# Optimization experiments

Measured on AMD Instinct MI355X. Metric: run time of the kernel, lower is better.

The kernel has to match this reference:

```python
import jax, jax.numpy as jnp
import numpy as np


def _conv3x3(x, w, b):
    # x: [B,C,H,W], w: [O,C,3,3], b: [O]; stride 1, padding 1 (SAME)
    y = jax.lax.conv_general_dilated(
        x, w, window_strides=(1, 1), padding='SAME',
        dimension_numbers=('NCHW', 'OIHW', 'NCHW'))
    return y + b[None, :, None, None]


def setup_inputs() -> dict:
    key = jax.random.key(0)
    ks = jax.random.split(key, 7)
    B, C, H, W = 8, 256, 48, 48
    emb = 512
    fan_out = emb * 9  # kaiming_normal_ fan_out, relu gain sqrt(2)
    std = float(np.sqrt(2.0 / fan_out))
    feat = jax.random.normal(ks[0], (B, C, H, W), dtype=jnp.float32)
    Wq = jax.random.normal(ks[1], (emb, C, 3, 3), dtype=jnp.float32) * std
    Wk = jax.random.normal(ks[2], (emb, C, 3, 3), dtype=jnp.float32) * std
    Wv = jax.random.normal(ks[3], (emb, C, 3, 3), dtype=jnp.float32) * std
    bound = 1.0 / np.sqrt(C * 9)
    bq = jax.random.uniform(ks[4], (emb,), jnp.float32, -bound, bound)
    bk = jax.random.uniform(ks[5], (emb,), jnp.float32, -bound, bound)
    bv = jax.random.uniform(ks[6], (emb,), jnp.float32, -bound, bound)
    return {"feat": feat, "Wq": Wq, "bq": bq, "Wk": Wk, "bk": bk, "Wv": Wv, "bv": bv}


def reference(feat, Wq, bq, Wk, bk, Wv, bv):
    B, C, H, W = feat.shape
    emb = Wq.shape[0]
    q = _conv3x3(feat, Wq, bq).reshape(B, emb, H * W)  # [B,E,N]
    k = _conv3x3(feat, Wk, bk).reshape(B, emb, H * W)
    v = _conv3x3(feat, Wv, bv).reshape(B, emb, H * W)
    # att[b,i,j] = <q[:, i], k[:, j]>, softmax over j (keys)
    att = jnp.einsum('bei,bej->bij', q, k)
    att = jax.nn.softmax(att, axis=2)
    # v_att[b,e,i] = sum_j v[b,e,j] * att[b,i,j]
    v_att = jnp.einsum('bej,bij->bei', v, att)
    return v_att.reshape(B, emb, H, W) + v.reshape(B, emb, H, W)
```

## Files before the change

### kernel.cpp

```cpp
#include <hip/hip_runtime.h>


typedef _Float16 f16;
typedef _Float16 f16x4 __attribute__((ext_vector_type(4)));
typedef _Float16 f16x8 __attribute__((ext_vector_type(8)));
typedef float    f32x4  __attribute__((ext_vector_type(4)));
typedef float    f32x16 __attribute__((ext_vector_type(16)));

__device__ __forceinline__ f32x16 mfma16(f16x8 a, f16x8 b, f32x16 c) {
  return __builtin_amdgcn_mfma_f32_32x32x16_f16(a, b, c, 0, 0, 0);
}

#define NB   8
#define NC   256
#define NH   48
#define NN   2304
#define NE   512
#define HP   50


__global__ void pack_feat(const float* __restrict__ x, f16* __restrict__ p) {
  int idx = blockIdx.x * 256 + threadIdx.x;
  int c  = idx & 255;
  int q  = idx >> 8;
  int xp = q % 50; int t = q / 50; int yp = t % 50; int b = t / 50;
  float v = 0.f;
  if (yp >= 1 && yp <= 48 && xp >= 1 && xp <= 48)
    v = x[((b * NC + c) * NH + (yp - 1)) * NH + (xp - 1)];
  p[idx] = (f16)v;
}

__global__ void pack_w(const float* __restrict__ wq, const float* __restrict__ wk,
                       const float* __restrict__ wv,
                       f16* __restrict__ oq, f16* __restrict__ ok,
                       f16* __restrict__ ov) {
  int idx = blockIdx.x * 256 + threadIdx.x;
  int c = idx & 255;
  int r = idx >> 8;
  int e = r & 511; int t = r >> 9;
  int src = (e * NC + c) * 9 + t;
  int cc = c >> 4, cl = c & 15, et = e >> 5, el = e & 31;
  int dst = ((cc * 9 + t) * 16 + et) * 512 + el * 16 + cl;
  oq[dst] = (f16)wq[src];
  ok[dst] = (f16)wk[src];
  ov[dst] = (f16)wv[src];
}

__global__ __launch_bounds__(256, 3) void conv3_all(
    const f16* __restrict__ xh,
    const f16* __restrict__ wq, const f16* __restrict__ wk,
    const f16* __restrict__ wv,
    const float* __restrict__ bq, const float* __restrict__ bk,
    const float* __restrict__ bv,
    f16* __restrict__ oq, f16* __restrict__ okf, f16* __restrict__ ovf) {
  __shared__ __align__(16) f16 sx[2][12000];

  const int tid = threadIdx.x;
  const int lane = tid & 63, wvx = tid >> 6;
  const int l31 = lane & 31;
  const int koff = (lane >> 5) * 8;
  const int et = blockIdx.x;
  const int e0 = et * 32;
  const int by = blockIdx.y;
  const int b = by / 6, strip = by % 6;
  const int y0 = strip * 8;
  const int F = blockIdx.z;
  const f16* w = (F == 0) ? wq : (F == 1) ? wk : wv;
  const float* bias = (F == 0) ? bq : (F == 1) ? bk : bv;

  int pb[3];
#pragma unroll
  for (int nt = 0; nt < 3; ++nt) {
    int n = wvx * 96 + nt * 32 + l31;
    pb[nt] = (n / 48) * 50 + (n % 48);
  }

  int sgp[4], sgo[4]; bool sok[4]; int gbase[4];
#pragma unroll
  for (int u = 0; u < 4; ++u) {
    int g = u * 256 + tid;
    sok[u] = (g < 1000);
    int gg = sok[u] ? g : 999;
    sgp[u] = gg >> 1; sgo[u] = (gg & 1) * 8;
    int row = sgp[u] / 50, xx = sgp[u] % 50;
    gbase[u] = ((b * HP + y0 + row) * HP + xx) * NC + sgo[u];
  }

  f32x16 acc[3];
#pragma unroll
  for (int nt = 0; nt < 3; ++nt)
#pragma unroll
    for (int i = 0; i < 16; ++i) acc[nt][i] = 0.f;

  const int wlocal = l31 * 16 + koff;

  {
    f16x8 rx0[4];
#pragma unroll
    for (int u = 0; u < 4; ++u)
      rx0[u] = *(const f16x8*)(xh + gbase[u]);
#pragma unroll
    for (int u = 0; u < 4; ++u)
      if (sok[u]) *(f16x8*)(sx[0] + sgp[u] * 24 + sgo[u]) = rx0[u];
  }
  __syncthreads();

  for (int cc = 0; cc < 16; ++cc) {
    f16x8 rx[4];
    if (cc < 15) {
      int c0 = (cc + 1) * 16;
#pragma unroll
      for (int u = 0; u < 4; ++u)
        rx[u] = *(const f16x8*)(xh + gbase[u] + c0);
    }
    const f16* sxc = sx[cc & 1];
    f16x8 wf = *(const f16x8*)(w + ((cc * 9 + 0) * 16 + et) * 512 + wlocal);
#pragma unroll
    for (int t = 0; t < 9; ++t) {
      f16x8 wcur = wf;
      if (t < 8)
        wf = *(const f16x8*)(w + ((cc * 9 + t + 1) * 16 + et) * 512 + wlocal);
      const int dy = t / 3, dx = t % 3;
      const int dpo = (dy * 50 + dx) * 24 + koff;
#pragma unroll
      for (int nt = 0; nt < 3; ++nt) {
        f16x8 bh = *(const f16x8*)(sxc + pb[nt] * 24 + dpo);
        acc[nt] = mfma16(wcur, bh, acc[nt]);
      }
    }
    if (cc < 15) {
#pragma unroll
      for (int u = 0; u < 4; ++u)
        if (sok[u]) *(f16x8*)(sx[(cc + 1) & 1] + sgp[u] * 24 + sgo[u]) = rx[u];
    }
    __syncthreads();
  }

  const int colh = (lane >> 5) * 4;
#pragma unroll
  for (int nt = 0; nt < 3; ++nt) {
    int n = wvx * 96 + nt * 32 + l31;
    int pos = (y0 + n / 48) * 48 + (n % 48);
    const int jblk = pos >> 5, jl = pos & 31;
    const int jc = pos >> 4, lhv = (pos >> 3) & 1, uv = pos & 7;
#pragma unroll
    for (int g = 0; g < 4; ++g) {
      int eb = e0 + g * 8 + colh;
      f32x4 sb = *(const f32x4*)(bias + eb);
      if (F == 0) {
        f16x4 hq;
#pragma unroll
        for (int j = 0; j < 4; ++j) hq[j] = (f16)(acc[nt][g * 4 + j] + sb[j]);
        *(f16x4*)(oq + ((size_t)b * NN + pos) * NE + eb) = hq;
      } else if (F == 1) {
        f16x4 hk;
#pragma unroll
        for (int j = 0; j < 4; ++j) hk[j] = (f16)(acc[nt][g * 4 + j] + sb[j]);
        *(f16x4*)(okf + ((((size_t)b * 72 + jblk) * 32 + (eb >> 4)) * 64 +
                         ((eb >> 3) & 1) * 32 + jl) * 8 + (eb & 7)) = hk;
      } else {
#pragma unroll
        for (int j = 0; j < 4; ++j) {
          int e = eb + j;
          ovf[((((size_t)b * 16 + (e >> 5)) * 144 + jc) * 64 + lhv * 32 + (e & 31)) * 8 + uv] =
              (f16)(acc[nt][g * 4 + j] + sb[j]);
        }
      }
    }
  }
}

__global__ __launch_bounds__(256, 3) void attn(
    const f16* __restrict__ qt, const f16* __restrict__ kf,
    const f16* __restrict__ vf, float* __restrict__ out) {
  __shared__ __align__(16) f16 q_lds[16384];
  __shared__ __align__(16) f16 sP2[4096];
  __shared__ __align__(16) float s_pmax[128];
  __shared__ __align__(16) float s_psum[128];

  const int tid = threadIdx.x;
  const int lane = tid & 63, wvx = tid >> 6;
  const int l31 = lane & 31, lh = lane >> 5;
  const int bid = blockIdx.x;
  const int b = bid & 7;
  const int i0 = (bid >> 3) * 32;

  {
    const f16* qb = qt + ((size_t)b * NN + i0) * NE;
#pragma unroll
    for (int it = 0; it < 8; ++it) {
      int g = it * 256 + tid;
      int row = g >> 6, gr = g & 63;
      f16x8 v = *(const f16x8*)(qb + row * NE + gr * 8);
      *(f16x8*)(q_lds + (gr >> 1) * 512 + (gr & 1) * 256 + row * 8) = v;
    }
  }
  __syncthreads();

  float m_reg = -1e30f, l_reg = 0.f;
  f32x16 O[4];
#pragma unroll
  for (int nt = 0; nt < 4; ++nt)
#pragma unroll
    for (int i = 0; i < 16; ++i) O[nt][i] = 0.f;

  const f16* kfw = kf + (size_t)(b * 72 + wvx) * 16384 + lane * 8;
  const f16* vfw = vf + (size_t)(b * 16 + wvx * 4) * 73728 + lane * 8;
  const f16* qlw = q_lds + lane * 8;

  for (int jt = 0; jt < 18; ++jt) {
    const f16* kfl = kfw + (size_t)jt * 4 * 16384;
    f32x16 S0, S1;
#pragma unroll
    for (int i = 0; i < 16; ++i) { S0[i] = 0.f; S1[i] = 0.f; }
    f16x8 kpipe[6];
#pragma unroll
    for (int t = 0; t < 6; ++t) kpipe[t] = *(const f16x8*)(kfl + t * 512);
#pragma unroll
    for (int c = 0; c < 32; ++c) {
      f16x8 ak = kpipe[c % 6];
      if (c + 6 < 32) kpipe[c % 6] = *(const f16x8*)(kfl + (c + 6) * 512);
      f16x8 aq = *(const f16x8*)(qlw + c * 512);
      if (c & 1) S1 = mfma16(ak, aq, S1);
      else       S0 = mfma16(ak, aq, S0);
    }
    f32x16 S;
#pragma unroll
    for (int r = 0; r < 16; ++r) S[r] = S0[r] + S1[r];

    float wmax = S[0];
#pragma unroll
    for (int r = 1; r < 16; ++r) wmax = fmaxf(wmax, S[r]);
    wmax = fmaxf(wmax, __shfl_xor(wmax, 32, 64));
    if (lane < 32) s_pmax[l31 * 4 + wvx] = wmax;
    __syncthreads();
    f32x4 pm4 = *(const f32x4*)(s_pmax + l31 * 4);
    float gmax = fmaxf(fmaxf(pm4[0], pm4[1]), fmaxf(pm4[2], pm4[3]));
    float mnew = fmaxf(m_reg, gmax);
    float alpha = __expf(m_reg - mnew);
    m_reg = mnew;

    f16 ph[16];
    float psum = 0.f;
#pragma unroll
    for (int r = 0; r < 16; ++r) {
      f16 p = (f16)__expf(S[r] - mnew);
      ph[r] = p;
      psum += (float)p;
    }
    union Q4 { f16x4 h; int i2[2]; };
    Q4 q4[4];
#pragma unroll
    for (int t = 0; t < 4; ++t)
#pragma unroll
      for (int u = 0; u < 4; ++u) q4[t].h[u] = ph[t * 4 + u];
#pragma unroll
    for (int ks = 0; ks < 2; ++ks) {
      Q4 t1, t2;
      t1.i2[0] = __shfl_xor(q4[2 * ks + 1].i2[0], 32, 64);
      t1.i2[1] = __shfl_xor(q4[2 * ks + 1].i2[1], 32, 64);
      t2.i2[0] = __shfl_xor(q4[2 * ks].i2[0], 32, 64);
      t2.i2[1] = __shfl_xor(q4[2 * ks].i2[1], 32, 64);
      f16x4 first  = lh ? t1.h : q4[2 * ks].h;
      f16x4 second = lh ? q4[2 * ks + 1].h : t2.h;
      f16x8 frag;
#pragma unroll
      for (int u = 0; u < 4; ++u) { frag[u] = first[u]; frag[4 + u] = second[u]; }
      *(f16x8*)(sP2 + ((wvx * 2 + ks) * 64 + lane) * 8) = frag;
    }
    psum += __shfl_xor(psum, 32, 64);
    if (lane < 32) s_psum[l31 * 4 + wvx] = psum;
#pragma unroll
    for (int nt = 0; nt < 4; ++nt)
#pragma unroll
      for (int r = 0; r < 16; ++r) O[nt][r] *= alpha;
    __syncthreads();
    f32x4 ps4 = *(const f32x4*)(s_psum + l31 * 4);
    l_reg = l_reg * alpha + (ps4[0] + ps4[1] + ps4[2] + ps4[3]);

    const f16* vfl = vfw + (size_t)jt * 8 * 512;
    f16x8 vpipe[6];
#pragma unroll
    for (int t = 0; t < 6; ++t) {
      int nt = t & 3, cg = t >> 2;
      vpipe[t] = *(const f16x8*)(vfl + (size_t)nt * 73728 + cg * 512);
    }
    f16x8 apc = *(const f16x8*)(sP2 + (0 * 64 + lane) * 8);
    f16x8 apn = *(const f16x8*)(sP2 + (1 * 64 + lane) * 8);
#pragma unroll
    for (int c = 0; c < 32; ++c) {
      int nt = c & 3, cg = c >> 2;
      f16x8 av = vpipe[c % 6];
      if (c + 6 < 32) {
        int nt2 = (c + 6) & 3, cg2 = (c + 6) >> 2;
        vpipe[c % 6] = *(const f16x8*)(vfl + (size_t)nt2 * 73728 + cg2 * 512);
      }
      O[nt] = mfma16(av, apc, O[nt]);
      if (nt == 3) {
        apc = apn;
        if (cg + 2 < 8) apn = *(const f16x8*)(sP2 + ((cg + 2) * 64 + lane) * 8);
      }
    }
  }

  float inv = 1.0f / l_reg;
  const int ii = i0 + l31;
  const int jcR = ii >> 4, lhR = (ii >> 3) & 1, uR = ii & 7;
#pragma unroll
  for (int nt = 0; nt < 4; ++nt) {
    const f16* vres = vf + ((((size_t)(b * 16 + wvx * 4 + nt)) * 144 + jcR) * 64 + lhR * 32) * 8 + uR;
    const int ebase = wvx * 128 + nt * 32;
#pragma unroll
    for (int r = 0; r < 16; ++r) {
      int el = (r & 3) + 8 * (r >> 2) + 4 * lh;
      float rv = (float)vres[el * 8];
      out[((size_t)b * NE + ebase + el) * NN + ii] = O[nt][r] * inv + rv;
    }
  }
}

extern "C" void kernel_launch(void* const* d_in, const int* in_sizes, int n_in,
                              void* d_out, int out_size, void* d_ws, size_t ws_size,
                              hipStream_t stream) {
  const float* feat = (const float*)d_in[0];
  const float* Wq = (const float*)d_in[1];
  const float* bq = (const float*)d_in[2];
  const float* Wk = (const float*)d_in[3];
  const float* bk = (const float*)d_in[4];
  const float* Wv = (const float*)d_in[5];
  const float* bv = (const float*)d_in[6];
  float* out = (float*)d_out;

  char* ws = (char*)d_ws;
  size_t off = 0;
  auto alloc = [&](size_t bytes) {
    void* p = ws + off;
    off += (bytes + 255) & ~(size_t)255;
    return p;
  };
  const size_t FP = (size_t)NB * HP * HP * NC;
  const size_t WP = (size_t)9 * NE * NC;
  const size_t QP = (size_t)NB * NN * NE;
  f16* fp  = (f16*)alloc(FP * 2);
  f16* wq  = (f16*)alloc(WP * 2);
  f16* wk  = (f16*)alloc(WP * 2);
  f16* wv  = (f16*)alloc(WP * 2);
  f16* q_t = (f16*)alloc(QP * 2);
  f16* k_f = (f16*)alloc(QP * 2);
  f16* v_f = (f16*)alloc(QP * 2);

  pack_feat<<<dim3(FP / 256), dim3(256), 0, stream>>>(feat, fp);
  pack_w<<<dim3(WP / 256), dim3(256), 0, stream>>>(Wq, Wk, Wv, wq, wk, wv);

  conv3_all<<<dim3(16, 48, 3), dim3(256), 0, stream>>>(
      fp, wq, wk, wv, bq, bk, bv, q_t, k_f, v_f);

  attn<<<dim3(576), dim3(256), 0, stream>>>(q_t, k_f, v_f, out);
}
```

Measured before the change: 443.8 us.

## Coalesce feature packing via LDS transpose, deepen K/V prefetch in attention

```diff
diff --git a/kernel.cpp b/kernel.cpp
--- a/kernel.cpp
+++ b/kernel.cpp
@@ -9,6 +9,13 @@
 
 __device__ __forceinline__ f32x16 mfma16(f16x8 a, f16x8 b, f32x16 c) {
   return __builtin_amdgcn_mfma_f32_32x32x16_f16(a, b, c, 0, 0, 0);
+}
+
+__device__ __forceinline__ f16x8 f16x8_zero() {
+  f16x8 z;
+#pragma unroll
+  for (int j = 0; j < 8; ++j) z[j] = (f16)0.f;
+  return z;
 }
 
 #define NB   8
@@ -20,14 +27,39 @@
 
 
 __global__ void pack_feat(const float* __restrict__ x, f16* __restrict__ p) {
-  int idx = blockIdx.x * 256 + threadIdx.x;
-  int c  = idx & 255;
-  int q  = idx >> 8;
-  int xp = q % 50; int t = q / 50; int yp = t % 50; int b = t / 50;
-  float v = 0.f;
-  if (yp >= 1 && yp <= 48 && xp >= 1 && xp <= 48)
-    v = x[((b * NC + c) * NH + (yp - 1)) * NH + (xp - 1)];
-  p[idx] = (f16)v;
+  __shared__ f16 tx[48 * 258];
+  const int b = blockIdx.x, yp = blockIdx.y;
+  const int tid = threadIdx.x;
+  f16* prow = p + ((size_t)(b * HP + yp) * HP) * NC;
+
+  if (yp == 0 || yp == HP - 1) {
+    for (int i = tid; i < 1600; i += 256)
+      *(f16x8*)(prow + i * 8) = f16x8_zero();
+    return;
+  }
+  const int y = yp - 1;
+#pragma unroll 4
+  for (int it = 0; it < 64; ++it) {
+    int i = it * 256 + tid;
+    int xsl = i & 63, c = i >> 6;
+    if (xsl < 48) {
+      float v = x[((b * NC + c) * NH + y) * NH + xsl];
+      tx[xsl * 258 + c] = (f16)v;
+    }
+  }
+  __syncthreads();
+#pragma unroll
+  for (int it = 0; it < 6; ++it) {
+    int xq = (tid >> 5) + it * 8;
+    int c0 = (tid & 31) * 8;
+    f16x8 v = *(const f16x8*)(tx + xq * 258 + c0);
+    *(f16x8*)(prow + (xq + 1) * NC + c0) = v;
+  }
+  if (tid < 64) {
+    int xp = (tid >> 5) * (HP - 1);
+    int c0 = (tid & 31) * 8;
+    *(f16x8*)(prow + xp * NC + c0) = f16x8_zero();
+  }
 }
 
 __global__ void pack_w(const float* __restrict__ wq, const float* __restrict__ wk,
@@ -106,6 +138,10 @@
   __syncthreads();
 
   for (int cc = 0; cc < 16; ++cc) {
+    f16x8 wreg[9];
+#pragma unroll
+    for (int t = 0; t < 9; ++t)
+      wreg[t] = *(const f16x8*)(w + ((cc * 9 + t) * 16 + et) * 512 + wlocal);
     f16x8 rx[4];
     if (cc < 15) {
       int c0 = (cc + 1) * 16;
@@ -114,18 +150,14 @@
         rx[u] = *(const f16x8*)(xh + gbase[u] + c0);
     }
     const f16* sxc = sx[cc & 1];
-    f16x8 wf = *(const f16x8*)(w + ((cc * 9 + 0) * 16 + et) * 512 + wlocal);
 #pragma unroll
     for (int t = 0; t < 9; ++t) {
-      f16x8 wcur = wf;
-      if (t < 8)
-        wf = *(const f16x8*)(w + ((cc * 9 + t + 1) * 16 + et) * 512 + wlocal);
       const int dy = t / 3, dx = t % 3;
       const int dpo = (dy * 50 + dx) * 24 + koff;
 #pragma unroll
       for (int nt = 0; nt < 3; ++nt) {
         f16x8 bh = *(const f16x8*)(sxc + pb[nt] * 24 + dpo);
-        acc[nt] = mfma16(wcur, bh, acc[nt]);
+        acc[nt] = mfma16(wreg[t], bh, acc[nt]);
       }
     }
     if (cc < 15) {
@@ -170,7 +202,7 @@
   }
 }
 
-__global__ __launch_bounds__(256, 3) void attn(
+__global__ __launch_bounds__(256, 2) void attn(
     const f16* __restrict__ qt, const f16* __restrict__ kf,
     const f16* __restrict__ vf, float* __restrict__ out) {
   __shared__ __align__(16) f16 q_lds[16384];
@@ -185,6 +217,9 @@
   const int b = bid & 7;
   const int i0 = (bid >> 3) * 32;
 
+  const f16* kfw = kf + (size_t)(b * 72 + wvx) * 16384 + lane * 8;
+  const f16* vfw = vf + (size_t)(b * 16 + wvx * 4) * 73728 + lane * 8;
+
   {
     const f16* qb = qt + ((size_t)b * NN + i0) * NE;
 #pragma unroll
@@ -195,6 +230,9 @@
       *(f16x8*)(q_lds + (gr >> 1) * 512 + (gr & 1) * 256 + row * 8) = v;
     }
   }
+  f16x8 kpipe[12];
+#pragma unroll
+  for (int t = 0; t < 12; ++t) kpipe[t] = *(const f16x8*)(kfw + t * 512);
   __syncthreads();
 
   float m_reg = -1e30f, l_reg = 0.f;
@@ -204,25 +242,28 @@
 #pragma unroll
     for (int i = 0; i < 16; ++i) O[nt][i] = 0.f;
 
-  const f16* kfw = kf + (size_t)(b * 72 + wvx) * 16384 + lane * 8;
-  const f16* vfw = vf + (size_t)(b * 16 + wvx * 4) * 73728 + lane * 8;
   const f16* qlw = q_lds + lane * 8;
+  f16x8 vpipe[12];
 
   for (int jt = 0; jt < 18; ++jt) {
     const f16* kfl = kfw + (size_t)jt * 4 * 16384;
+    const f16* vfl = vfw + (size_t)jt * 8 * 512;
+
     f32x16 S0, S1;
 #pragma unroll
     for (int i = 0; i < 16; ++i) { S0[i] = 0.f; S1[i] = 0.f; }
-    f16x8 kpipe[6];
-#pragma unroll
-    for (int t = 0; t < 6; ++t) kpipe[t] = *(const f16x8*)(kfl + t * 512);
 #pragma unroll
     for (int c = 0; c < 32; ++c) {
-      f16x8 ak = kpipe[c % 6];
-      if (c + 6 < 32) kpipe[c % 6] = *(const f16x8*)(kfl + (c + 6) * 512);
+      f16x8 ak = kpipe[c % 12];
+      if (c + 12 < 32) kpipe[c % 12] = *(const f16x8*)(kfl + (c + 12) * 512);
       f16x8 aq = *(const f16x8*)(qlw + c * 512);
       if (c & 1) S1 = mfma16(ak, aq, S1);
       else       S0 = mfma16(ak, aq, S0);
+    }
+#pragma unroll
+    for (int t = 0; t < 12; ++t) {
+      int nt = t & 3, cg = t >> 2;
+      vpipe[t] = *(const f16x8*)(vfl + (size_t)nt * 73728 + cg * 512);
     }
     f32x16 S;
 #pragma unroll
@@ -278,22 +319,20 @@
     f32x4 ps4 = *(const f32x4*)(s_psum + l31 * 4);
     l_reg = l_reg * alpha + (ps4[0] + ps4[1] + ps4[2] + ps4[3]);
 
-    const f16* vfl = vfw + (size_t)jt * 8 * 512;
-    f16x8 vpipe[6];
-#pragma unroll
-    for (int t = 0; t < 6; ++t) {
-      int nt = t & 3, cg = t >> 2;
-      vpipe[t] = *(const f16x8*)(vfl + (size_t)nt * 73728 + cg * 512);
+    if (jt < 17) {
+      const f16* kn = kfw + (size_t)(jt + 1) * 4 * 16384;
+#pragma unroll
+      for (int t = 0; t < 12; ++t) kpipe[t] = *(const f16x8*)(kn + t * 512);
     }
     f16x8 apc = *(const f16x8*)(sP2 + (0 * 64 + lane) * 8);
     f16x8 apn = *(const f16x8*)(sP2 + (1 * 64 + lane) * 8);
 #pragma unroll
     for (int c = 0; c < 32; ++c) {
       int nt = c & 3, cg = c >> 2;
-      f16x8 av = vpipe[c % 6];
-      if (c + 6 < 32) {
-        int nt2 = (c + 6) & 3, cg2 = (c + 6) >> 2;
-        vpipe[c % 6] = *(const f16x8*)(vfl + (size_t)nt2 * 73728 + cg2 * 512);
+      f16x8 av = vpipe[c % 12];
+      if (c + 12 < 32) {
+        int c2 = c + 12, nt2 = c2 & 3, cg2 = c2 >> 2;
+        vpipe[c % 12] = *(const f16x8*)(vfl + (size_t)nt2 * 73728 + cg2 * 512);
       }
       O[nt] = mfma16(av, apc, O[nt]);
       if (nt == 3) {
@@ -349,7 +388,7 @@
   f16* k_f = (f16*)alloc(QP * 2);
   f16* v_f = (f16*)alloc(QP * 2);
 
-  pack_feat<<<dim3(FP / 256), dim3(256), 0, stream>>>(feat, fp);
+  pack_feat<<<dim3(NB, HP), dim3(256), 0, stream>>>(feat, fp);
   pack_w<<<dim3(WP / 256), dim3(256), 0, stream>>>(Wq, Wk, Wv, wq, wk, wv);
 
   conv3_all<<<dim3(16, 48, 3), dim3(256), 0, stream>>>(
```

Result: faster. 434.9 us (-2.0%).
